# Kernel tuning notes

Measured on AMD Instinct MI355X. Metric: run time of the kernel, lower is better.

The kernel has to match this reference:

```python
import jax, jax.numpy as jnp
from jax import lax
import numpy as np

RADIUS = 2  # init kwarg; radius>1 enables avg_pool2d(kernel=2r-1, stride=1, pad=r-1)
EPS = 1e-6


def setup_inputs() -> dict:
    key = jax.random.key(0)
    ks = jax.random.split(key, 5)
    B, C, H, W = 32, 3, 512, 512
    x = jax.random.normal(ks[0], (B, C, H, W), dtype=jnp.float32)
    w1 = jax.random.normal(ks[1], (32, 6), dtype=jnp.float32) * 0.4
    b1 = jax.random.normal(ks[2], (32,), dtype=jnp.float32) * 0.1
    w2 = jax.random.normal(ks[3], (64, 32), dtype=jnp.float32) * 0.18
    b2 = jax.random.normal(ks[4], (64,), dtype=jnp.float32) * 0.1
    return {"x": x, "w1": w1, "b1": b1, "w2": w2, "b2": b2}


def _depthwise_conv(x, k2d):
    # x: [B,3,H,W]; k2d: [3,3] stencil applied per channel (cross-correlation, zero-pad SAME)
    kern = jnp.tile(k2d[None, None], (3, 1, 1, 1))  # [out=3, in/group=1, 3, 3]
    return lax.conv_general_dilated(
        x, kern, window_strides=(1, 1), padding="SAME",
        dimension_numbers=("NCHW", "OIHW", "NCHW"), feature_group_count=3)


def _avg_pool_same(x, k):
    # avg_pool2d(kernel=k, stride=1, padding=(k-1)//2, count_include_pad=True)
    p = (k - 1) // 2
    s = lax.reduce_window(x, jnp.array(0, x.dtype), lax.add,
                          (1, 1, k, k), (1, 1, 1, 1),
                          [(0, 0), (0, 0), (p, p), (p, p)])
    return s / jnp.asarray(k * k, x.dtype)


def reference(x, w1, b1, w2, b2):
    sob_x = jnp.array([[1., 0., -1.], [2., 0., -2.], [1., 0., -1.]], dtype=x.dtype)
    sob_y = sob_x.T
    gx = _depthwise_conv(x, sob_x)
    gy = _depthwise_conv(x, sob_y)
    mag = jnp.sqrt(gx * gx + gy * gy + EPS)  # [B,3,H,W]
    if RADIUS > 1:
        mag = _avg_pool_same(mag, 2 * RADIUS - 1)
    mean = jnp.mean(mag, axis=(2, 3))                 # [B,3]
    std = jnp.std(mag, axis=(2, 3), ddof=1)           # torch .std() is unbiased
    feats = jnp.stack([mean, std], axis=2).reshape(x.shape[0], 6)  # [m0,s0,m1,s1,m2,s2]
    h = jax.nn.relu(feats @ w1.T + b1)
    return h @ w2.T + b2
```

## Files before the change

kernel.cpp:

```cpp
#include <hip/hip_runtime.h>
#include <math.h>


__global__ __launch_bounds__(256) void sobel_pool_stats(
    const float* __restrict__ x, double* __restrict__ parts) {
  const int tid = threadIdx.x;
  const int lane = tid & 63;
  const int w = tid >> 6;
  const int bc = blockIdx.y;
  const int chunk = blockIdx.x * 4 + w;
  const int row0 = chunk * 12;

  const float* __restrict__ xb = x + (size_t)bc * (512 * 512) + lane * 8;

  auto load8 = [&](int r, float* o) {
    if ((unsigned)r < 512u) {
      const float* p = xb + (size_t)r * 512;
      float4 u = *(const float4*)(p);
      float4 v = *(const float4*)(p + 4);
      o[0] = u.x; o[1] = u.y; o[2] = u.z; o[3] = u.w;
      o[4] = v.x; o[5] = v.y; o[6] = v.z; o[7] = v.w;
    } else {
#pragma unroll
      for (int k = 0; k < 8; ++k) o[k] = 0.f;
    }
  };

  float S[8], X[8];
  {
    float t0[8], t1[8];
    load8(row0 - 2, t0);
    load8(row0 - 1, t1);
#pragma unroll
    for (int k = 0; k < 8; ++k) { S[k] = t0[k] + t1[k]; X[k] = t1[k]; }
  }

  auto magstep = [&](int rm, float* mg) {
    float xn[8], S2[8], a[8], b[8];
    load8(rm + 1, xn);
#pragma unroll
    for (int k = 0; k < 8; ++k) S2[k] = X[k] + xn[k];
#pragma unroll
    for (int k = 0; k < 8; ++k) { a[k] = S[k] + S2[k]; b[k] = S[k] - S2[k]; }
    float aL = __shfl_up(a[7], 1), aR = __shfl_down(a[0], 1);
    float bL = __shfl_up(b[7], 1), bR = __shfl_down(b[0], 1);
    if (lane == 0)  { aL = 0.f; bL = 0.f; }
    if (lane == 63) { aR = 0.f; bR = 0.f; }
    const float rmask = ((unsigned)rm < 512u) ? 1.f : 0.f;
#pragma unroll
    for (int j = 0; j < 8; ++j) {
      float am = j ? a[j - 1] : aL;
      float ap = (j < 7) ? a[j + 1] : aR;
      float bm = j ? b[j - 1] : bL;
      float bp = (j < 7) ? b[j + 1] : bR;
      float gx = am - ap;
      float gy = fmaf(2.f, b[j], bm + bp);
      float m2 = fmaf(gx, gx, 1e-6f);
      m2 = fmaf(gy, gy, m2);
      mg[j] = __builtin_amdgcn_sqrtf(m2) * rmask;
    }
#pragma unroll
    for (int k = 0; k < 8; ++k) { S[k] = S2[k]; X[k] = xn[k]; }
  };

  float MM[8], MC[8], MP[8];
  magstep(row0 - 1, MM);
  magstep(row0, MC);

  float s = 0.f, ss = 0.f;
#pragma unroll
  for (int i = 0; i < 12; ++i) {
    magstep(row0 + 1 + i, MP);
    if ((unsigned)(row0 + i) < 512u) {
      float cs[8];
#pragma unroll
      for (int k = 0; k < 8; ++k) cs[k] = (MM[k] + MP[k]) + MC[k];
      float csL = __shfl_up(cs[7], 1), csR = __shfl_down(cs[0], 1);
      if (lane == 0) csL = 0.f;
      if (lane == 63) csR = 0.f;
#pragma unroll
      for (int j = 0; j < 8; ++j) {
        float cm = j ? cs[j - 1] : csL;
        float cp = (j < 7) ? cs[j + 1] : csR;
        float t = (cm + cp) + cs[j];
        s += t;
        ss = fmaf(t, t, ss);
      }
    }
#pragma unroll
    for (int k = 0; k < 8; ++k) { MM[k] = MC[k]; MC[k] = MP[k]; }
  }

  double ds = (double)s * (1.0 / 9.0);
  double dss = (double)ss * (1.0 / 81.0);
  for (int off = 32; off > 0; off >>= 1) {
    ds += __shfl_down(ds, off);
    dss += __shfl_down(dss, off);
  }
  if (lane == 0) {
    size_t idx = ((size_t)bc * 44 + chunk) * 2;
    parts[idx] = ds;
    parts[idx + 1] = dss;
  }
}

__global__ __launch_bounds__(256) void stats_mlp(
    const double* __restrict__ parts,
    const float* __restrict__ w1, const float* __restrict__ b1,
    const float* __restrict__ w2, const float* __restrict__ b2,
    float* __restrict__ out) {
  __shared__ float feats[32 * 6];
  __shared__ float hbuf[32 * 32];
  const int tid = threadIdx.x;

  if (tid < 96) {
    int b = tid / 3;
    int ch = tid - b * 3;
    double s = 0.0, ss = 0.0;
    const double* p = parts + (size_t)tid * 88;
#pragma unroll
    for (int t = 0; t < 44; ++t) {
      s += p[2 * t];
      ss += p[2 * t + 1];
    }
    const double N = 262144.0;
    double mean = s / N;
    double var = (ss - s * s / N) / (N - 1.0);
    if (var < 0.0) var = 0.0;
    feats[b * 6 + 2 * ch] = (float)mean;
    feats[b * 6 + 2 * ch + 1] = (float)sqrt(var);
  }
  __syncthreads();

  for (int idx = tid; idx < 32 * 32; idx += 256) {
    int i = idx >> 5, j = idx & 31;
    float acc = b1[j];
#pragma unroll
    for (int k = 0; k < 6; ++k) acc += feats[i * 6 + k] * w1[j * 6 + k];
    hbuf[idx] = acc > 0.f ? acc : 0.f;
  }
  __syncthreads();

  for (int idx = tid; idx < 2048; idx += 256) {
    int i = idx >> 6, o = idx & 63;
    float acc = b2[o];
#pragma unroll
    for (int j = 0; j < 32; ++j) acc += hbuf[i * 32 + j] * w2[o * 32 + j];
    out[idx] = acc;
  }
}

extern "C" void kernel_launch(void* const* d_in, const int* in_sizes, int n_in,
                              void* d_out, int out_size, void* d_ws, size_t ws_size,
                              hipStream_t stream) {
  const float* x = (const float*)d_in[0];
  const float* w1 = (const float*)d_in[1];
  const float* b1 = (const float*)d_in[2];
  const float* w2 = (const float*)d_in[3];
  const float* b2 = (const float*)d_in[4];
  float* out = (float*)d_out;
  double* parts = (double*)d_ws;

  dim3 grid(11, 96);
  sobel_pool_stats<<<grid, 256, 0, stream>>>(x, parts);
  stats_mlp<<<1, 256, 0, stream>>>(parts, w1, b1, w2, b2, out);
}
```

Measured before the change: 33.17 us.

## Shrink row chunks, double-buffer row loads, and branch-skip out-of-range rows

Cuts the rows per wave from 12 to 8, which raises the grid from 11 to 16 blocks per channel and removes the wasted tail rows that 44 chunks of 12 produced (528 rows for 512). Row loads are now issued one step ahead into a double buffer so global latency overlaps the Sobel and pool arithmetic. The magnitude buffers rotate by index instead of being copied each step, out-of-range rows skip the Sobel math through a branch, and the per-row bounds check in the pooling loop is dropped because every row is now in range. In exchange there is more halo re-reading per output row and more partial sums for the reduction kernel to add up.

```diff
diff --git a/kernel.cpp b/kernel.cpp
--- a/kernel.cpp
+++ b/kernel.cpp
@@ -9,7 +9,7 @@
   const int w = tid >> 6;
   const int bc = blockIdx.y;
   const int chunk = blockIdx.x * 4 + w;
-  const int row0 = chunk * 12;
+  const int row0 = chunk * 8;
 
   const float* __restrict__ xb = x + (size_t)bc * (512 * 512) + lane * 8;
 
@@ -35,60 +35,70 @@
     for (int k = 0; k < 8; ++k) { S[k] = t0[k] + t1[k]; X[k] = t1[k]; }
   }
 
-  auto magstep = [&](int rm, float* mg) {
-    float xn[8], S2[8], a[8], b[8];
-    load8(rm + 1, xn);
+  auto magstep = [&](const float* xn, int rm, float* mg) {
+    float S2[8];
 #pragma unroll
     for (int k = 0; k < 8; ++k) S2[k] = X[k] + xn[k];
+    if ((unsigned)rm < 512u) {
+      float a[8], b[8];
 #pragma unroll
-    for (int k = 0; k < 8; ++k) { a[k] = S[k] + S2[k]; b[k] = S[k] - S2[k]; }
-    float aL = __shfl_up(a[7], 1), aR = __shfl_down(a[0], 1);
-    float bL = __shfl_up(b[7], 1), bR = __shfl_down(b[0], 1);
-    if (lane == 0)  { aL = 0.f; bL = 0.f; }
-    if (lane == 63) { aR = 0.f; bR = 0.f; }
-    const float rmask = ((unsigned)rm < 512u) ? 1.f : 0.f;
+      for (int k = 0; k < 8; ++k) { a[k] = S[k] + S2[k]; b[k] = S[k] - S2[k]; }
+      float aL = __shfl_up(a[7], 1), aR = __shfl_down(a[0], 1);
+      float bL = __shfl_up(b[7], 1), bR = __shfl_down(b[0], 1);
+      if (lane == 0)  { aL = 0.f; bL = 0.f; }
+      if (lane == 63) { aR = 0.f; bR = 0.f; }
 #pragma unroll
-    for (int j = 0; j < 8; ++j) {
-      float am = j ? a[j - 1] : aL;
-      float ap = (j < 7) ? a[j + 1] : aR;
-      float bm = j ? b[j - 1] : bL;
-      float bp = (j < 7) ? b[j + 1] : bR;
-      float gx = am - ap;
-      float gy = fmaf(2.f, b[j], bm + bp);
-      float m2 = fmaf(gx, gx, 1e-6f);
-      m2 = fmaf(gy, gy, m2);
-      mg[j] = __builtin_amdgcn_sqrtf(m2) * rmask;
+      for (int j = 0; j < 8; ++j) {
+        float am = j ? a[j - 1] : aL;
+        float ap = (j < 7) ? a[j + 1] : aR;
+        float bm = j ? b[j - 1] : bL;
+        float bp = (j < 7) ? b[j + 1] : bR;
+        float gx = am - ap;
+        float gy = fmaf(2.f, b[j], bm + bp);
+        float m2 = fmaf(gx, gx, 1e-6f);
+        m2 = fmaf(gy, gy, m2);
+        mg[j] = __builtin_amdgcn_sqrtf(m2);
+      }
+    } else {
+#pragma unroll
+      for (int j = 0; j < 8; ++j) mg[j] = 0.f;
     }
 #pragma unroll
     for (int k = 0; k < 8; ++k) { S[k] = S2[k]; X[k] = xn[k]; }
   };
 
-  float MM[8], MC[8], MP[8];
-  magstep(row0 - 1, MM);
-  magstep(row0, MC);
+  float M[3][8], xnb[2][8];
+  load8(row0, xnb[0]);
+  load8(row0 + 1, xnb[1]);
+  magstep(xnb[0], row0 - 1, M[0]);
+  load8(row0 + 2, xnb[0]);
+  magstep(xnb[1], row0, M[1]);
 
   float s = 0.f, ss = 0.f;
 #pragma unroll
-  for (int i = 0; i < 12; ++i) {
-    magstep(row0 + 1 + i, MP);
-    if ((unsigned)(row0 + i) < 512u) {
-      float cs[8];
+  for (int i = 0; i < 8; ++i) {
+    float* cur = xnb[i & 1];
+    float* nxt = xnb[(i & 1) ^ 1];
+    if (i < 7) load8(row0 + 3 + i, nxt);
+    float* MM = M[i % 3];
+    float* MC = M[(i + 1) % 3];
+    float* MP = M[(i + 2) % 3];
+    magstep(cur, row0 + 1 + i, MP);
+
+    float cs[8];
 #pragma unroll
-      for (int k = 0; k < 8; ++k) cs[k] = (MM[k] + MP[k]) + MC[k];
-      float csL = __shfl_up(cs[7], 1), csR = __shfl_down(cs[0], 1);
-      if (lane == 0) csL = 0.f;
-      if (lane == 63) csR = 0.f;
+    for (int k = 0; k < 8; ++k) cs[k] = (MM[k] + MP[k]) + MC[k];
+    float csL = __shfl_up(cs[7], 1), csR = __shfl_down(cs[0], 1);
+    if (lane == 0) csL = 0.f;
+    if (lane == 63) csR = 0.f;
 #pragma unroll
-      for (int j = 0; j < 8; ++j) {
-        float cm = j ? cs[j - 1] : csL;
-        float cp = (j < 7) ? cs[j + 1] : csR;
-        float t = (cm + cp) + cs[j];
-        s += t;
-        ss = fmaf(t, t, ss);
-      }
+    for (int j = 0; j < 8; ++j) {
+      float cm = j ? cs[j - 1] : csL;
+      float cp = (j < 7) ? cs[j + 1] : csR;
+      float t = (cm + cp) + cs[j];
+      s += t;
+      ss = fmaf(t, t, ss);
     }
-#pragma unroll
-    for (int k = 0; k < 8; ++k) { MM[k] = MC[k]; MC[k] = MP[k]; }
   }
 
   double ds = (double)s * (1.0 / 9.0);
@@ -98,7 +108,7 @@
     dss += __shfl_down(dss, off);
   }
   if (lane == 0) {
-    size_t idx = ((size_t)bc * 44 + chunk) * 2;
+    size_t idx = ((size_t)bc * 64 + chunk) * 2;
     parts[idx] = ds;
     parts[idx + 1] = dss;
   }
@@ -117,9 +127,9 @@
     int b = tid / 3;
     int ch = tid - b * 3;
     double s = 0.0, ss = 0.0;
-    const double* p = parts + (size_t)tid * 88;
+    const double* p = parts + (size_t)tid * 128;
 #pragma unroll
-    for (int t = 0; t < 44; ++t) {
+    for (int t = 0; t < 64; ++t) {
       s += p[2 * t];
       ss += p[2 * t + 1];
     }
@@ -161,7 +171,7 @@
   float* out = (float*)d_out;
   double* parts = (double*)d_ws;
 
-  dim3 grid(11, 96);
+  dim3 grid(16, 96);
   sobel_pool_stats<<<grid, 256, 0, stream>>>(x, parts);
   stats_mlp<<<1, 256, 0, stream>>>(parts, w1, b1, w2, b2, out);
 }
```

After: 38.66 us. +16.6%, slower.
